# Kernel tuning notes

Hardware: AMD Instinct MI355X
Metric: run time of the kernel (lower is better)

The kernel has to match this reference:

```python
import jax, jax.numpy as jnp
import numpy as np

NEG_SLOPE = 0.2
BN_EPS = 1e-5


def _gatv2(x, Wl, Wr, att, b, src, dst, N):
    # PyG GATv2Conv, concat=False: lin_l on source, lin_r on target,
    # e = a^T LeakyReLU(x_l[j] + x_r[i]); softmax over incoming edges of i;
    # out = mean_h( sum_j alpha_ij * x_l[j] ) + bias
    H, C = att.shape
    xl = (x @ Wl).reshape(N, H, C)
    xr = (x @ Wr).reshape(N, H, C)
    e = jax.nn.leaky_relu(xl[src] + xr[dst], NEG_SLOPE)          # [E,H,C]
    score = jnp.einsum('ehc,hc->eh', e, att)                     # [E,H]
    m = jax.ops.segment_max(score, dst, num_segments=N)          # [N,H]
    a = jnp.exp(score - m[dst])
    denom = jax.ops.segment_sum(a, dst, num_segments=N)
    alpha = a / denom[dst]                                       # [E,H]
    out = jax.ops.segment_sum(alpha[..., None] * xl[src], dst, num_segments=N)  # [N,H,C]
    return out.mean(axis=1) + b


def _bn(h, g, be):
    # BatchNorm1d, training-mode statistics (biased variance)
    mu = h.mean(axis=0)
    var = h.var(axis=0)
    return g * (h - mu) * jax.lax.rsqrt(var + BN_EPS) + be


def _gelu(x):
    return jax.nn.gelu(x, approximate=False)


def setup_inputs() -> dict:
    key = jax.random.key(0)
    N, F, HID, LAT, H, E, G = 50000, 64, 64, 64, 4, 800000, 256
    ks = jax.random.split(key, 32)
    d = {}
    d['x'] = jax.random.normal(ks[0], (N, F), dtype=jnp.float32)
    d['edge_src'] = jax.random.randint(ks[1], (E,), 0, N, dtype=jnp.int32)
    d['edge_dst'] = jax.random.randint(ks[2], (E,), 0, N, dtype=jnp.int32)
    d['batch'] = jnp.sort(jax.random.randint(ks[3], (N,), 0, G, dtype=jnp.int32))
    d['num_graphs'] = G
    def lin(k, fi, fo):
        return jax.random.normal(k, (fi, fo), dtype=jnp.float32) / np.sqrt(fi)
    i = 4
    for L, fin in zip((1, 2, 3), (F, HID, HID)):
        d[f'Wl{L}'] = lin(ks[i], fin, H * HID); i += 1
        d[f'Wr{L}'] = lin(ks[i], fin, H * HID); i += 1
        d[f'att{L}'] = jax.random.normal(ks[i], (H, HID), dtype=jnp.float32) / np.sqrt(HID); i += 1
        d[f'b{L}'] = jnp.zeros((HID,), dtype=jnp.float32)
        d[f'g{L}'] = jax.random.uniform(ks[i], (HID,), dtype=jnp.float32, minval=0.5, maxval=1.5); i += 1
        d[f'be{L}'] = 0.1 * jax.random.normal(ks[i], (HID,), dtype=jnp.float32); i += 1
    d['Wmu'] = lin(ks[i], HID, LAT); i += 1
    d['bmu'] = jnp.zeros((LAT,), dtype=jnp.float32)
    d['Wlv'] = lin(ks[i], HID, LAT); i += 1
    d['blv'] = jnp.zeros((LAT,), dtype=jnp.float32)
    return d


def reference(x, edge_src, edge_dst, batch, num_graphs,
              Wl1, Wr1, att1, b1, g1, be1,
              Wl2, Wr2, att2, b2, g2, be2,
              Wl3, Wr3, att3, b3, g3, be3,
              Wmu, bmu, Wlv, blv):
    N = x.shape[0]
    loops = jnp.arange(N, dtype=edge_src.dtype)
    src = jnp.concatenate([edge_src, loops])  # add_self_loops=True (PyG default)
    dst = jnp.concatenate([edge_dst, loops])

    h = _gelu(_bn(_gatv2(x, Wl1, Wr1, att1, b1, src, dst, N), g1, be1))
    h_in = h
    h = _gelu(_bn(_gatv2(h, Wl2, Wr2, att2, b2, src, dst, N), g2, be2)) + h_in
    h_in = h
    h = _gelu(_bn(_gatv2(h, Wl3, Wr3, att3, b3, src, dst, N), g3, be3)) + h_in

    h_pool = jax.ops.segment_sum(h, batch, num_segments=num_graphs)  # global_add_pool
    return (h_pool @ Wmu + bmu, h_pool @ Wlv + blv)
```

## Files before the change

kernel.cpp:

```cpp
#include <hip/hip_runtime.h>
#include <math.h>

typedef __attribute__((ext_vector_type(8))) short bf16x8;
typedef __attribute__((ext_vector_type(4))) float f32x4;
typedef __attribute__((ext_vector_type(2))) float f32x2;

static __device__ __forceinline__ unsigned short f2bf(float f) {
  unsigned u = __float_as_uint(f);
  unsigned r = (u + 0x7FFF + ((u >> 16) & 1)) >> 16;
  return (unsigned short)r;
}

#define DPP_ADD(x, ctrl) \
  ((x) + __int_as_float(__builtin_amdgcn_update_dpp(0, __float_as_int(x), (ctrl), 0xf, 0xf, true)))

#define NSHARD 64
#define NEB 256
#define ECAP 6144


__global__ __launch_bounds__(256) void k_prep(const float* __restrict__ W0, const float* __restrict__ W1,
                                              const float* __restrict__ W2, const float* __restrict__ W3,
                                              const float* __restrict__ W4, const float* __restrict__ W5,
                                              unsigned short* __restrict__ wt,
                                              const int* __restrict__ esrc,
                                              const int* __restrict__ edst,
                                              int* __restrict__ bktcnt,
                                              int2* __restrict__ ebuf, int E, int N) {
  if (blockIdx.x < 384) {
    int gid = blockIdx.x * 256 + threadIdx.x;
    int m = gid >> 14;
    int r = gid & 16383;
    int k = r >> 8;
    int n = r & 255;
    const float* W = (m == 0) ? W0 : (m == 1) ? W1 : (m == 2) ? W2
                   : (m == 3) ? W3 : (m == 4) ? W4 : W5;
    wt[(size_t)m * 16384 + n * 64 + k] = f2bf(W[k * 256 + n]);
    return;
  }
  const int b = blockIdx.x - 384;
  const int nbk = (N + 255) >> 8;
  __shared__ int cnt[256], base[256];
  cnt[threadIdx.x] = 0;
  __syncthreads();
  const int chunk = (E + NEB - 1) / NEB;
  const int e0 = b * chunk, e1 = min(e0 + chunk, E);
  for (int e = e0 + threadIdx.x; e < e1; e += 256) atomicAdd(&cnt[edst[e] >> 8], 1);
  __syncthreads();
  if (threadIdx.x < nbk && cnt[threadIdx.x])
    base[threadIdx.x] = atomicAdd(&bktcnt[threadIdx.x], cnt[threadIdx.x]);
  cnt[threadIdx.x] = 0;
  __syncthreads();
  for (int e = e0 + threadIdx.x; e < e1; e += 256) {
    int d = edst[e];
    int bk = d >> 8;
    int p = base[bk] + atomicAdd(&cnt[bk], 1);
    ebuf[(size_t)bk * ECAP + p] = make_int2(d, esrc[e]);
  }
}


static __device__ __forceinline__ void csr_pass2(const int2* __restrict__ ebuf,
                                                 const int* __restrict__ bktcnt,
                                                 int* __restrict__ rowptr,
                                                 int* __restrict__ colb,
                                                 int* __restrict__ ccur,
                                                 int N, char* smem) {
  const int b = blockIdx.x;
  const int nbk = (N + 255) >> 8;
  if (b >= nbk) return;
  int* hist = (int*)smem;
  int* s = (int*)smem + 256;
  int* sb = (int*)smem + 512;
  const int tid = threadIdx.x;
  const int lo = b * ECAP;
  const int hi = lo + bktcnt[b];
  hist[tid] = 0;
  __syncthreads();
  for (int i = lo + tid; i < hi; i += 256) atomicAdd(&hist[ebuf[i].x & 255], 1);
  __syncthreads();
  int deg = hist[tid];
  int pd = (deg + 3) & ~3;
  s[tid] = pd;
  __syncthreads();
  for (int off = 1; off < 256; off <<= 1) {
    int t = (tid >= off) ? s[tid - off] : 0;
    __syncthreads();
    s[tid] += t;
    __syncthreads();
  }
  if (tid == 255) sb[0] = atomicAdd(ccur, s[255]);
  __syncthreads();
  int pos = sb[0] + s[tid] - pd;
  int node = (b << 8) + tid;
  if (node < N) rowptr[node] = (int)((unsigned)pos | ((unsigned)deg << 22));
  hist[tid] = pos;
  __syncthreads();
  for (int i = lo + tid; i < hi; i += 256) {
    int2 e = ebuf[i];
    int p = atomicAdd(&hist[e.x & 255], 1);
    colb[p] = e.y << 8;
  }
}


static __device__ __forceinline__ void mm_gemm(const float* __restrict__ src,
                                               const float* __restrict__ bnsums,
                                               const float* __restrict__ g,
                                               const float* __restrict__ be,
                                               const float* __restrict__ resid,
                                               float* __restrict__ hout,
                                               const unsigned short* __restrict__ wt,
                                               unsigned char* __restrict__ xlb,
                                               unsigned char* __restrict__ xrb,
                                               int N, int ntiles, float inv_n,
                                               char* smem) {
  unsigned short* Bs = (unsigned short*)smem;
  unsigned short* Ah = (unsigned short*)(smem + 32768);
  const int t = threadIdx.x;
  const unsigned short* wb = wt + (blockIdx.y ? 16384 : 0);
  unsigned char* dst = blockIdx.y ? xrb : xlb;

  const int wave = t >> 6, lane = t & 63;
  const int rw = (wave & 1) * 16, cw = (wave >> 1) * 128;
  const int m15 = lane & 15, quad = lane >> 4;
  const int arow = t >> 3, ac0 = (t & 7) * 8;
  const int aoff = arow * 64 + (((t & 7) ^ (arow & 7)) << 3);

  float scale[8], shift[8];
  if (bnsums) {
    float* stat = (float*)smem;
    if (t < 128) {
      float a = 0.f;
#pragma unroll
      for (int sd = 0; sd < NSHARD; ++sd) a += bnsums[sd * 128 + t];
      stat[t] = a;
    }
    __syncthreads();
#pragma unroll
    for (int i = 0; i < 8; ++i) {
      int c = ac0 + i;
      float mu = stat[c] * inv_n;
      float var = stat[64 + c] * inv_n - mu * mu;
      float rs = rsqrtf(var + 1e-5f) * g[c];
      scale[i] = rs;
      shift[i] = be[c] - mu * rs;
    }
    __syncthreads();
  }

#pragma unroll
  for (int j = 0; j < 8; ++j) {
    int cidx = t + 256 * j;
    int n = cidx >> 3, gg = cidx & 7;
    *(bf16x8*)&Bs[n * 64 + (((gg ^ ((n >> 3) & 7))) << 3)] =
        *(const bf16x8*)(wb + (size_t)n * 64 + gg * 8);
  }

  const bool wr_h = (hout != nullptr) && (blockIdx.y == 0);
  const int gstride = gridDim.x;

  float4 a0, a1, rv0, rv1;
  auto loadA = [&](int tl, float4& x0, float4& x1, float4& r0v, float4& r1v) {
    x0 = make_float4(0.f, 0.f, 0.f, 0.f);
    x1 = make_float4(0.f, 0.f, 0.f, 0.f);
    r0v = make_float4(0.f, 0.f, 0.f, 0.f);
    r1v = make_float4(0.f, 0.f, 0.f, 0.f);
    int gr = tl * 32 + arow;
    if (tl < ntiles && gr < N) {
      x0 = *(const float4*)(src + (size_t)gr * 64 + ac0);
      x1 = *(const float4*)(src + (size_t)gr * 64 + ac0 + 4);
      if (resid) {
        r0v = *(const float4*)(resid + (size_t)gr * 64 + ac0);
        r1v = *(const float4*)(resid + (size_t)gr * 64 + ac0 + 4);
      }
    }
  };
  loadA(blockIdx.x, a0, a1, rv0, rv1);

  for (int tile = blockIdx.x; tile < ntiles; tile += gstride) {
    int r0 = tile * 32;
    int gr = r0 + arow;
    {
      float vs[8] = {a0.x, a0.y, a0.z, a0.w, a1.x, a1.y, a1.z, a1.w};
      if (bnsums) {
        float rv[8] = {rv0.x, rv0.y, rv0.z, rv0.w, rv1.x, rv1.y, rv1.z, rv1.w};
#pragma unroll
        for (int i = 0; i < 8; ++i) {
          float v = fmaf(vs[i], scale[i], shift[i]);
          float ge = 0.5f * v * (1.f + erff(v * 0.70710678118654752f));
          vs[i] = ge + rv[i];
        }
        if (wr_h && gr < N) {
          float4 o0 = {vs[0], vs[1], vs[2], vs[3]};
          float4 o1 = {vs[4], vs[5], vs[6], vs[7]};
          *(float4*)(hout + (size_t)gr * 64 + ac0) = o0;
          *(float4*)(hout + (size_t)gr * 64 + ac0 + 4) = o1;
        }
      }
      bf16x8 hi8;
#pragma unroll
      for (int i = 0; i < 8; ++i) hi8[i] = (short)f2bf(vs[i]);
      *(bf16x8*)&Ah[aoff] = hi8;
    }
    __syncthreads();

    loadA(tile + gstride, a0, a1, rv0, rv1);

    f32x4 acc[8];
#pragma unroll
    for (int s = 0; s < 8; ++s) acc[s] = (f32x4){0.f, 0.f, 0.f, 0.f};
    const int xq = m15 & 7;
#pragma unroll
    for (int kk = 0; kk < 64; kk += 32) {
      const int ga = (((kk >> 3) + quad) ^ xq) << 3;
      bf16x8 ah = *(const bf16x8*)&Ah[(rw + m15) * 64 + ga];
#pragma unroll
      for (int s = 0; s < 8; ++s) {
        bf16x8 b = *(const bf16x8*)&Bs[(cw + m15 * 8 + s) * 64 + ga];
        acc[s] = __builtin_amdgcn_mfma_f32_16x16x32_bf16(ah, b, acc[s], 0, 0, 0);
      }
    }
#pragma unroll
    for (int r = 0; r < 4; ++r) {
      int row_g = r0 + rw + quad * 4 + r;
      if (row_g < N) {
        int w0 = __builtin_amdgcn_cvt_pk_fp8_f32(acc[0][r], acc[1][r], 0, false);
        w0 = __builtin_amdgcn_cvt_pk_fp8_f32(acc[2][r], acc[3][r], w0, true);
        int w1 = __builtin_amdgcn_cvt_pk_fp8_f32(acc[4][r], acc[5][r], 0, false);
        w1 = __builtin_amdgcn_cvt_pk_fp8_f32(acc[6][r], acc[7][r], w1, true);
        uint2 o = {(unsigned)w0, (unsigned)w1};
        *(uint2*)(dst + (size_t)row_g * 256 + cw + m15 * 8) = o;
      }
    }
    __syncthreads();
  }
}

__global__ __launch_bounds__(256, 4) void k_mm0(const float* __restrict__ src,
                                                const unsigned short* __restrict__ wt,
                                                unsigned char* __restrict__ xlb,
                                                unsigned char* __restrict__ xrb,
                                                const int2* __restrict__ ebuf,
                                                const int* __restrict__ bktcnt,
                                                int* __restrict__ rowptr,
                                                int* __restrict__ colb,
                                                int* __restrict__ ccur,
                                                int N, int ntiles) {
  __shared__ __align__(16) char smem[36864];
  if (blockIdx.y == 2) {
    csr_pass2(ebuf, bktcnt, rowptr, colb, ccur, N, smem);
    return;
  }
  mm_gemm(src, nullptr, nullptr, nullptr, nullptr, nullptr, wt, xlb, xrb, N, ntiles, 0.f, smem);
}

__global__ __launch_bounds__(256, 4) void k_mm1(const float* __restrict__ src,
                                                const float* __restrict__ bnsums,
                                                const float* __restrict__ g,
                                                const float* __restrict__ be,
                                                float* __restrict__ hout,
                                                const unsigned short* __restrict__ wt,
                                                unsigned char* __restrict__ xlb,
                                                unsigned char* __restrict__ xrb,
                                                int N, int ntiles, float inv_n) {
  __shared__ __align__(16) char smem[36864];
  mm_gemm(src, bnsums, g, be, nullptr, hout, wt, xlb, xrb, N, ntiles, inv_n, smem);
}

__global__ __launch_bounds__(256, 4) void k_mm2(const float* __restrict__ src,
                                                const float* __restrict__ bnsums,
                                                const float* __restrict__ g,
                                                const float* __restrict__ be,
                                                const float* __restrict__ resid,
                                                float* __restrict__ hout,
                                                const unsigned short* __restrict__ wt,
                                                unsigned char* __restrict__ xlb,
                                                unsigned char* __restrict__ xrb,
                                                int N, int ntiles, float inv_n) {
  __shared__ __align__(16) char smem[36864];
  mm_gemm(src, bnsums, g, be, resid, hout, wt, xlb, xrb, N, ntiles, inv_n, smem);
}


static __device__ __forceinline__ void gat_body(const unsigned char* __restrict__ xlb,
                                                const unsigned char* __restrict__ xrb,
                                                const float* __restrict__ att,
                                                const float* __restrict__ bias,
                                                const int* __restrict__ rowptr,
                                                const int* __restrict__ colb,
                                                float* __restrict__ out,
                                                float* __restrict__ bnsums, int N) {
  __shared__ float sres[4][64];
  const int lane = threadIdx.x & 63;
  const int wv = threadIdx.x >> 6;
  const int node0 = blockIdx.x * 4 + wv;
  const bool valid = node0 < N;
  const int node = __builtin_amdgcn_readfirstlane(valid ? node0 : 0);
  const int rp = rowptr[node];
  const int beg = rp & 0x3FFFFF;
  const int deg = (int)(((unsigned)rp) >> 22);
  const int end = valid ? beg + deg : beg;

  const unsigned char* xl = xlb;
  const unsigned lb = (unsigned)lane * 4u;

  int4 c0 = *(const int4*)(colb + beg);
  int4 c1 = *(const int4*)(colb + beg + 4);
  unsigned vbs = *(const unsigned*)(xl + ((unsigned)(node << 8) + lb));
  unsigned d0 = *(const unsigned*)(xl + ((unsigned)c0.x + lb));
  unsigned d1 = *(const unsigned*)(xl + ((unsigned)c0.y + lb));
  unsigned d2 = *(const unsigned*)(xl + ((unsigned)c0.z + lb));
  unsigned d3 = *(const unsigned*)(xl + ((unsigned)c0.w + lb));
  unsigned t0 = *(const unsigned*)(xl + ((unsigned)c1.x + lb));
  unsigned t1 = *(const unsigned*)(xl + ((unsigned)c1.y + lb));
  unsigned t2 = *(const unsigned*)(xl + ((unsigned)c1.z + lb));
  unsigned t3 = *(const unsigned*)(xl + ((unsigned)c1.w + lb));
  int4 cn = *(const int4*)(colb + beg + 8);

  float4 a4 = *(const float4*)(att + lane * 4);
  const float LOG2E = 1.4426950408889634f;
  const f32x2 a01 = {a4.x * LOG2E, a4.y * LOG2E};
  const f32x2 a23 = {a4.z * LOG2E, a4.w * LOG2E};
  const f32x2 c02 = {0.2f, 0.2f};
  unsigned xru = *(const unsigned*)(xrb + ((unsigned)(node << 8) + lb));
  const f32x2 xr01 = __builtin_amdgcn_cvt_pk_f32_fp8((int)xru, false);
  const f32x2 xr23 = __builtin_amdgcn_cvt_pk_f32_fp8((int)xru, true);
  const f32x2 sv01 = __builtin_amdgcn_cvt_pk_f32_fp8((int)vbs, false);
  const f32x2 sv23 = __builtin_amdgcn_cvt_pk_f32_fp8((int)vbs, true);

  float m;
  {
    f32x2 s01 = sv01 + xr01;
    f32x2 s23 = sv23 + xr23;
    s01 = __builtin_elementwise_max(s01, s01 * c02);
    s23 = __builtin_elementwise_max(s23, s23 * c02);
    f32x2 q = __builtin_elementwise_fma(s23, a23, s01 * a01);
    float p = q.x + q.y;
    p = DPP_ADD(p, 0xB1);
    p = DPP_ADD(p, 0x4E);
    p = DPP_ADD(p, 0x124);
    p = DPP_ADD(p, 0x128);
    m = p;
  }
  float lsum = 1.f;
  f32x2 o01 = sv01, o23 = sv23;

  auto proc = [&](unsigned vb, bool ok) {
    f32x2 v01 = __builtin_amdgcn_cvt_pk_f32_fp8((int)vb, false);
    f32x2 v23 = __builtin_amdgcn_cvt_pk_f32_fp8((int)vb, true);
    f32x2 s01 = v01 + xr01;
    f32x2 s23 = v23 + xr23;
    s01 = __builtin_elementwise_max(s01, s01 * c02);
    s23 = __builtin_elementwise_max(s23, s23 * c02);
    f32x2 q = __builtin_elementwise_fma(s23, a23, s01 * a01);
    float p = q.x + q.y;
    p = DPP_ADD(p, 0xB1);
    p = DPP_ADD(p, 0x4E);
    p = DPP_ADD(p, 0x124);
    p = DPP_ADD(p, 0x128);
    float w = __builtin_amdgcn_exp2f(fminf(p - m, 126.f));
    w = ok ? w : 0.f;
    lsum += w;
    f32x2 w2 = {w, w};
    o01 = __builtin_elementwise_fma(w2, v01, o01);
    o23 = __builtin_elementwise_fma(w2, v23, o23);
  };

  for (int e = beg; e < end; e += 4) {
    unsigned u0 = *(const unsigned*)(xl + ((unsigned)cn.x + lb));
    unsigned u1 = *(const unsigned*)(xl + ((unsigned)cn.y + lb));
    unsigned u2 = *(const unsigned*)(xl + ((unsigned)cn.z + lb));
    unsigned u3 = *(const unsigned*)(xl + ((unsigned)cn.w + lb));
    cn = *(const int4*)(colb + e + 12);
    proc(d0, true);
    proc(d1, e + 1 < end);
    proc(d2, e + 2 < end);
    proc(d3, e + 3 < end);
    d0 = t0; d1 = t1; d2 = t2; d3 = t3;
    t0 = u0; t1 = u1; t2 = u2; t3 = u3;
  }

  float inv = __builtin_amdgcn_rcpf(lsum);
  float rx = o01.x * inv, ry = o01.y * inv, rz = o23.x * inv, rw2 = o23.y * inv;
  rx += __shfl_xor(rx, 16, 64); rx += __shfl_xor(rx, 32, 64);
  ry += __shfl_xor(ry, 16, 64); ry += __shfl_xor(ry, 32, 64);
  rz += __shfl_xor(rz, 16, 64); rz += __shfl_xor(rz, 32, 64);
  rw2 += __shfl_xor(rw2, 16, 64); rw2 += __shfl_xor(rw2, 32, 64);
  if (lane < 16) {
    float4 res = {0.f, 0.f, 0.f, 0.f};
    if (valid) {
      float4 b4 = *(const float4*)(bias + lane * 4);
      res.x = 0.25f * rx + b4.x;
      res.y = 0.25f * ry + b4.y;
      res.z = 0.25f * rz + b4.z;
      res.w = 0.25f * rw2 + b4.w;
      *(float4*)(out + (size_t)node * 64 + lane * 4) = res;
    }
    *(float4*)&sres[wv][lane * 4] = res;
  }
  __syncthreads();
  if (threadIdx.x < 64) {
    int c = threadIdx.x;
    float s0 = sres[0][c], s1 = sres[1][c], s2 = sres[2][c], s3 = sres[3][c];
    float* bs = bnsums + (size_t)(blockIdx.x & (NSHARD - 1)) * 128;
    atomicAdd(&bs[c], s0 + s1 + s2 + s3);
    atomicAdd(&bs[64 + c], s0 * s0 + s1 * s1 + s2 * s2 + s3 * s3);
  }
}

__global__ __launch_bounds__(256) void k_gat0(const unsigned char* __restrict__ xlb,
                                              const unsigned char* __restrict__ xrb,
                                              const float* __restrict__ att,
                                              const float* __restrict__ bias,
                                              const int* __restrict__ rowptr,
                                              const int* __restrict__ colb,
                                              float* __restrict__ out,
                                              float* __restrict__ bnsums, int N) {
  gat_body(xlb, xrb, att, bias, rowptr, colb, out, bnsums, N);
}
__global__ __launch_bounds__(256) void k_gat1(const unsigned char* __restrict__ xlb,
                                              const unsigned char* __restrict__ xrb,
                                              const float* __restrict__ att,
                                              const float* __restrict__ bias,
                                              const int* __restrict__ rowptr,
                                              const int* __restrict__ colb,
                                              float* __restrict__ out,
                                              float* __restrict__ bnsums, int N) {
  gat_body(xlb, xrb, att, bias, rowptr, colb, out, bnsums, N);
}
__global__ __launch_bounds__(256) void k_gat2(const unsigned char* __restrict__ xlb,
                                              const unsigned char* __restrict__ xrb,
                                              const float* __restrict__ att,
                                              const float* __restrict__ bias,
                                              const int* __restrict__ rowptr,
                                              const int* __restrict__ colb,
                                              float* __restrict__ out,
                                              float* __restrict__ bnsums, int N) {
  gat_body(xlb, xrb, att, bias, rowptr, colb, out, bnsums, N);
}


__global__ __launch_bounds__(256) void k_bn_pool(const float* __restrict__ gat,
                                                 const float* __restrict__ bnsums,
                                                 const float* __restrict__ g,
                                                 const float* __restrict__ be,
                                                 const float* __restrict__ resid,
                                                 const int* __restrict__ batch,
                                                 float* __restrict__ pool,
                                                 int N, float inv_n) {
  __shared__ float sc[64], sh[64];
  if (threadIdx.x < 64) {
    int c = threadIdx.x;
    float s = 0.f, q = 0.f;
    for (int sd = 0; sd < NSHARD; ++sd) {
      s += bnsums[sd * 128 + c];
      q += bnsums[sd * 128 + 64 + c];
    }
    float mu = s * inv_n;
    float var = q * inv_n - mu * mu;
    float rs = rsqrtf(var + 1e-5f) * g[c];
    sc[c] = rs;
    sh[c] = be[c] - mu * rs;
  }
  __syncthreads();
  const int c = threadIdx.x & 63;
  const int wv = threadIdx.x >> 6;
  int n0 = (blockIdx.x * 4 + wv) * 32;
  if (n0 >= N) return;
  int n1 = min(n0 + 32, N);
  int curg = batch[n0];
  float acc = 0.f;
  for (int n = n0; n < n1; ++n) {
    int b = batch[n];
    if (b != curg) {
      atomicAdd(&pool[(size_t)curg * 64 + c], acc);
      acc = 0.f;
      curg = b;
    }
    float v = fmaf(gat[(size_t)n * 64 + c], sc[c], sh[c]);
    float ge = 0.5f * v * (1.f + erff(v * 0.70710678118654752f));
    acc += ge + resid[(size_t)n * 64 + c];
  }
  atomicAdd(&pool[(size_t)curg * 64 + c], acc);
}


__global__ void k_head(const float* __restrict__ pool, const float* __restrict__ Wmu,
                       const float* __restrict__ bmu, const float* __restrict__ Wlv,
                       const float* __restrict__ blv, float* __restrict__ out, int G) {
  int g = blockIdx.x;
  int c = threadIdx.x;
  __shared__ float row[64];
  row[c] = pool[(size_t)g * 64 + c];
  __syncthreads();
  float am = 0.f, al = 0.f;
  for (int k = 0; k < 64; ++k) {
    float r = row[k];
    am = fmaf(r, Wmu[k * 64 + c], am);
    al = fmaf(r, Wlv[k * 64 + c], al);
  }
  out[(size_t)g * 64 + c] = am + bmu[c];
  out[(size_t)G * 64 + (size_t)g * 64 + c] = al + blv[c];
}


extern "C" void kernel_launch(void* const* d_in, const int* in_sizes, int n_in,
                              void* d_out, int out_size, void* d_ws, size_t ws_size,
                              hipStream_t stream) {
  const float* x    = (const float*)d_in[0];
  const int* esrc   = (const int*)d_in[1];
  const int* edst   = (const int*)d_in[2];
  const int* batch  = (const int*)d_in[3];
  const float* Wl[3]  = {(const float*)d_in[5],  (const float*)d_in[11], (const float*)d_in[17]};
  const float* Wr[3]  = {(const float*)d_in[6],  (const float*)d_in[12], (const float*)d_in[18]};
  const float* att[3] = {(const float*)d_in[7],  (const float*)d_in[13], (const float*)d_in[19]};
  const float* bia[3] = {(const float*)d_in[8],  (const float*)d_in[14], (const float*)d_in[20]};
  const float* gam[3] = {(const float*)d_in[9],  (const float*)d_in[15], (const float*)d_in[21]};
  const float* bet[3] = {(const float*)d_in[10], (const float*)d_in[16], (const float*)d_in[22]};
  const float* Wmu = (const float*)d_in[23];
  const float* bmu = (const float*)d_in[24];
  const float* Wlv = (const float*)d_in[25];
  const float* blv = (const float*)d_in[26];
  float* out = (float*)d_out;

  const int N = in_sizes[0] / 64;
  const int E = in_sizes[1];
  const int G = out_size / 128;
  const int nbk = (N + 255) / 256;

  char* p = (char*)d_ws;
  auto alloc = [&](size_t bytes) -> void* {
    void* r = (void*)p;
    p += (bytes + 255) & ~(size_t)255;
    return r;
  };
  int*   bktcnt  = (int*)alloc(256 * 4);
  float* bnsums  = (float*)alloc(3 * NSHARD * 128 * 4);
  float* pool    = (float*)alloc((size_t)G * 64 * 4);
  int*   ccur    = (int*)alloc(256);
  int*   colb    = (int*)alloc(((size_t)E + 3 * (size_t)N + 64) * 4);
  char*  zend    = p;
  unsigned char* xlb = (unsigned char*)alloc((size_t)N * 256);
  unsigned char* xrb = (unsigned char*)alloc((size_t)N * 256);
  float* hA     = (float*)alloc((size_t)N * 64 * 4);
  float* hB     = (float*)alloc((size_t)N * 64 * 4);
  float* gat    = (float*)alloc((size_t)N * 64 * 4);
  int*   rowptr = (int*)alloc((size_t)(N + 1) * 4);
  int2*  ebuf   = (int2*)alloc((size_t)nbk * ECAP * 8);
  unsigned short* wt = (unsigned short*)alloc(6 * 16384 * 2);

  const int nbGat = (N + 3) / 4;
  const int ntiles = (N + 31) / 32;
  const float inv_n = 1.f / (float)N;

  hipMemsetAsync(bktcnt, 0, (size_t)(zend - (char*)bktcnt), stream);

  k_prep<<<384 + NEB, 256, 0, stream>>>(Wl[0], Wr[0], Wl[1], Wr[1], Wl[2], Wr[2], wt,
                                        esrc, edst, bktcnt, ebuf, E, N);

  float* bns0 = bnsums;
  float* bns1 = bnsums + NSHARD * 128;
  float* bns2 = bnsums + 2 * NSHARD * 128;

  k_mm0<<<dim3(512, 3), 256, 0, stream>>>(x, wt, xlb, xrb, ebuf, bktcnt, rowptr, colb,
                                          ccur, N, ntiles);
  k_gat0<<<nbGat, 256, 0, stream>>>(xlb, xrb, att[0], bia[0], rowptr, colb, gat, bns0, N);
  k_mm1<<<dim3(512, 2), 256, 0, stream>>>(gat, bns0, gam[0], bet[0], hA,
                                          wt + 2 * 16384, xlb, xrb, N, ntiles, inv_n);
  k_gat1<<<nbGat, 256, 0, stream>>>(xlb, xrb, att[1], bia[1], rowptr, colb, gat, bns1, N);
  k_mm2<<<dim3(512, 2), 256, 0, stream>>>(gat, bns1, gam[1], bet[1], hA, hB,
                                          wt + 4 * 16384, xlb, xrb, N, ntiles, inv_n);
  k_gat2<<<nbGat, 256, 0, stream>>>(xlb, xrb, att[2], bia[2], rowptr, colb, gat, bns2, N);
  k_bn_pool<<<(N + 127) / 128, 256, 0, stream>>>(gat, bns2, gam[2], bet[2], hB, batch, pool,
                                                 N, inv_n);
  k_head<<<G, 64, 0, stream>>>(pool, Wmu, bmu, Wlv, blv, out, G);
}
```

Measured before the change: 365.1 us.

## Split GAT aggregation wave into two half-waves each handling alternate edges

The GAT gather kernel now has each 32-lane half of a wavefront process a different edge, with every lane holding 8 fp8 features (uint2 loads) instead of 4. This halves the number of serial per-edge score/exp/FMA steps per wave and shortens the per-head reduction by one DPP step, at the cost of more registers per lane, an extra cross-half merge of lsum and outputs, and a longer final shuffle reduction. Masking uses per-half edge validity, and the self-loop term is counted only in the lower half.

```diff
diff --git a/kernel.cpp b/kernel.cpp
--- a/kernel.cpp
+++ b/kernel.cpp
@@ -294,6 +294,8 @@
   __shared__ float sres[4][64];
   const int lane = threadIdx.x & 63;
   const int wv = threadIdx.x >> 6;
+  const int half = lane >> 5;
+  const int l5 = lane & 31;
   const int node0 = blockIdx.x * 4 + wv;
   const bool valid = node0 < N;
   const int node = __builtin_amdgcn_readfirstlane(valid ? node0 : 0);
@@ -303,101 +305,117 @@
   const int end = valid ? beg + deg : beg;
 
   const unsigned char* xl = xlb;
-  const unsigned lb = (unsigned)lane * 4u;
+  const unsigned lb = (unsigned)l5 * 8u;
+
+  auto sel = [&](int a, int b) { return (unsigned)(half ? b : a); };
 
   int4 c0 = *(const int4*)(colb + beg);
   int4 c1 = *(const int4*)(colb + beg + 4);
-  unsigned vbs = *(const unsigned*)(xl + ((unsigned)(node << 8) + lb));
-  unsigned d0 = *(const unsigned*)(xl + ((unsigned)c0.x + lb));
-  unsigned d1 = *(const unsigned*)(xl + ((unsigned)c0.y + lb));
-  unsigned d2 = *(const unsigned*)(xl + ((unsigned)c0.z + lb));
-  unsigned d3 = *(const unsigned*)(xl + ((unsigned)c0.w + lb));
-  unsigned t0 = *(const unsigned*)(xl + ((unsigned)c1.x + lb));
-  unsigned t1 = *(const unsigned*)(xl + ((unsigned)c1.y + lb));
-  unsigned t2 = *(const unsigned*)(xl + ((unsigned)c1.z + lb));
-  unsigned t3 = *(const unsigned*)(xl + ((unsigned)c1.w + lb));
+  const unsigned self_off = (unsigned)(node << 8);
+  uint2 vbs = *(const uint2*)(xl + self_off + lb);
+  uint2 pd0 = *(const uint2*)(xl + (sel(c0.x, c0.y) + lb));
+  uint2 pd1 = *(const uint2*)(xl + (sel(c0.z, c0.w) + lb));
+  uint2 pt0 = *(const uint2*)(xl + (sel(c1.x, c1.y) + lb));
+  uint2 pt1 = *(const uint2*)(xl + (sel(c1.z, c1.w) + lb));
   int4 cn = *(const int4*)(colb + beg + 8);
 
-  float4 a4 = *(const float4*)(att + lane * 4);
+  float4 aa = *(const float4*)(att + l5 * 8);
+  float4 ab = *(const float4*)(att + l5 * 8 + 4);
   const float LOG2E = 1.4426950408889634f;
-  const f32x2 a01 = {a4.x * LOG2E, a4.y * LOG2E};
-  const f32x2 a23 = {a4.z * LOG2E, a4.w * LOG2E};
+  const f32x2 a01 = {aa.x * LOG2E, aa.y * LOG2E};
+  const f32x2 a23 = {aa.z * LOG2E, aa.w * LOG2E};
+  const f32x2 a45 = {ab.x * LOG2E, ab.y * LOG2E};
+  const f32x2 a67 = {ab.z * LOG2E, ab.w * LOG2E};
   const f32x2 c02 = {0.2f, 0.2f};
-  unsigned xru = *(const unsigned*)(xrb + ((unsigned)(node << 8) + lb));
-  const f32x2 xr01 = __builtin_amdgcn_cvt_pk_f32_fp8((int)xru, false);
-  const f32x2 xr23 = __builtin_amdgcn_cvt_pk_f32_fp8((int)xru, true);
-  const f32x2 sv01 = __builtin_amdgcn_cvt_pk_f32_fp8((int)vbs, false);
-  const f32x2 sv23 = __builtin_amdgcn_cvt_pk_f32_fp8((int)vbs, true);
-
-  float m;
-  {
-    f32x2 s01 = sv01 + xr01;
-    f32x2 s23 = sv23 + xr23;
+  uint2 xru = *(const uint2*)(xrb + self_off + lb);
+  const f32x2 xr01 = __builtin_amdgcn_cvt_pk_f32_fp8((int)xru.x, false);
+  const f32x2 xr23 = __builtin_amdgcn_cvt_pk_f32_fp8((int)xru.x, true);
+  const f32x2 xr45 = __builtin_amdgcn_cvt_pk_f32_fp8((int)xru.y, false);
+  const f32x2 xr67 = __builtin_amdgcn_cvt_pk_f32_fp8((int)xru.y, true);
+
+  auto score = [&](uint2 vb, f32x2& v01, f32x2& v23, f32x2& v45, f32x2& v67) -> float {
+    v01 = __builtin_amdgcn_cvt_pk_f32_fp8((int)vb.x, false);
+    v23 = __builtin_amdgcn_cvt_pk_f32_fp8((int)vb.x, true);
+    v45 = __builtin_amdgcn_cvt_pk_f32_fp8((int)vb.y, false);
+    v67 = __builtin_amdgcn_cvt_pk_f32_fp8((int)vb.y, true);
+    f32x2 s01 = v01 + xr01;
+    f32x2 s23 = v23 + xr23;
+    f32x2 s45 = v45 + xr45;
+    f32x2 s67 = v67 + xr67;
     s01 = __builtin_elementwise_max(s01, s01 * c02);
     s23 = __builtin_elementwise_max(s23, s23 * c02);
-    f32x2 q = __builtin_elementwise_fma(s23, a23, s01 * a01);
+    s45 = __builtin_elementwise_max(s45, s45 * c02);
+    s67 = __builtin_elementwise_max(s67, s67 * c02);
+    f32x2 q = s01 * a01;
+    q = __builtin_elementwise_fma(s23, a23, q);
+    q = __builtin_elementwise_fma(s45, a45, q);
+    q = __builtin_elementwise_fma(s67, a67, q);
     float p = q.x + q.y;
     p = DPP_ADD(p, 0xB1);
     p = DPP_ADD(p, 0x4E);
-    p = DPP_ADD(p, 0x124);
-    p = DPP_ADD(p, 0x128);
-    m = p;
-  }
-  float lsum = 1.f;
-  f32x2 o01 = sv01, o23 = sv23;
-
-  auto proc = [&](unsigned vb, bool ok) {
-    f32x2 v01 = __builtin_amdgcn_cvt_pk_f32_fp8((int)vb, false);
-    f32x2 v23 = __builtin_amdgcn_cvt_pk_f32_fp8((int)vb, true);
-    f32x2 s01 = v01 + xr01;
-    f32x2 s23 = v23 + xr23;
-    s01 = __builtin_elementwise_max(s01, s01 * c02);
-    s23 = __builtin_elementwise_max(s23, s23 * c02);
-    f32x2 q = __builtin_elementwise_fma(s23, a23, s01 * a01);
-    float p = q.x + q.y;
-    p = DPP_ADD(p, 0xB1);
-    p = DPP_ADD(p, 0x4E);
-    p = DPP_ADD(p, 0x124);
-    p = DPP_ADD(p, 0x128);
+    p = DPP_ADD(p, 0x141);
+    return p;
+  };
+
+  f32x2 sv01, sv23, sv45, sv67;
+  const float m = score(vbs, sv01, sv23, sv45, sv67);
+
+  const float hsel = half ? 0.f : 1.f;
+  float lsum = hsel;
+  const f32x2 hs2 = {hsel, hsel};
+  f32x2 o01 = sv01 * hs2, o23 = sv23 * hs2, o45 = sv45 * hs2, o67 = sv67 * hs2;
+
+  auto proc = [&](uint2 vb, int ebase) {
+    f32x2 v01, v23, v45, v67;
+    float p = score(vb, v01, v23, v45, v67);
     float w = __builtin_amdgcn_exp2f(fminf(p - m, 126.f));
-    w = ok ? w : 0.f;
+    w = (ebase + half < end) ? w : 0.f;
     lsum += w;
     f32x2 w2 = {w, w};
     o01 = __builtin_elementwise_fma(w2, v01, o01);
     o23 = __builtin_elementwise_fma(w2, v23, o23);
+    o45 = __builtin_elementwise_fma(w2, v45, o45);
+    o67 = __builtin_elementwise_fma(w2, v67, o67);
   };
 
   for (int e = beg; e < end; e += 4) {
-    unsigned u0 = *(const unsigned*)(xl + ((unsigned)cn.x + lb));
-    unsigned u1 = *(const unsigned*)(xl + ((unsigned)cn.y + lb));
-    unsigned u2 = *(const unsigned*)(xl + ((unsigned)cn.z + lb));
-    unsigned u3 = *(const unsigned*)(xl + ((unsigned)cn.w + lb));
+    uint2 pu0 = *(const uint2*)(xl + (sel(cn.x, cn.y) + lb));
+    uint2 pu1 = *(const uint2*)(xl + (sel(cn.z, cn.w) + lb));
     cn = *(const int4*)(colb + e + 12);
-    proc(d0, true);
-    proc(d1, e + 1 < end);
-    proc(d2, e + 2 < end);
-    proc(d3, e + 3 < end);
-    d0 = t0; d1 = t1; d2 = t2; d3 = t3;
-    t0 = u0; t1 = u1; t2 = u2; t3 = u3;
-  }
-
+    proc(pd0, e);
+    proc(pd1, e + 2);
+    pd0 = pt0; pd1 = pt1;
+    pt0 = pu0; pt1 = pu1;
+  }
+
+  lsum += __shfl_xor(lsum, 32, 64);
   float inv = __builtin_amdgcn_rcpf(lsum);
-  float rx = o01.x * inv, ry = o01.y * inv, rz = o23.x * inv, rw2 = o23.y * inv;
-  rx += __shfl_xor(rx, 16, 64); rx += __shfl_xor(rx, 32, 64);
-  ry += __shfl_xor(ry, 16, 64); ry += __shfl_xor(ry, 32, 64);
-  rz += __shfl_xor(rz, 16, 64); rz += __shfl_xor(rz, 32, 64);
-  rw2 += __shfl_xor(rw2, 16, 64); rw2 += __shfl_xor(rw2, 32, 64);
-  if (lane < 16) {
-    float4 res = {0.f, 0.f, 0.f, 0.f};
+  float r[8] = {o01.x * inv, o01.y * inv, o23.x * inv, o23.y * inv,
+                o45.x * inv, o45.y * inv, o67.x * inv, o67.y * inv};
+#pragma unroll
+  for (int j = 0; j < 8; ++j) {
+    r[j] += __shfl_xor(r[j], 8, 64);
+    r[j] += __shfl_xor(r[j], 16, 64);
+    r[j] += __shfl_xor(r[j], 32, 64);
+  }
+  if (lane < 8) {
+    float4 res0 = {0.f, 0.f, 0.f, 0.f}, res1 = {0.f, 0.f, 0.f, 0.f};
     if (valid) {
-      float4 b4 = *(const float4*)(bias + lane * 4);
-      res.x = 0.25f * rx + b4.x;
-      res.y = 0.25f * ry + b4.y;
-      res.z = 0.25f * rz + b4.z;
-      res.w = 0.25f * rw2 + b4.w;
-      *(float4*)(out + (size_t)node * 64 + lane * 4) = res;
-    }
-    *(float4*)&sres[wv][lane * 4] = res;
+      float4 b0 = *(const float4*)(bias + lane * 8);
+      float4 b1 = *(const float4*)(bias + lane * 8 + 4);
+      res0.x = 0.25f * r[0] + b0.x;
+      res0.y = 0.25f * r[1] + b0.y;
+      res0.z = 0.25f * r[2] + b0.z;
+      res0.w = 0.25f * r[3] + b0.w;
+      res1.x = 0.25f * r[4] + b1.x;
+      res1.y = 0.25f * r[5] + b1.y;
+      res1.z = 0.25f * r[6] + b1.z;
+      res1.w = 0.25f * r[7] + b1.w;
+      *(float4*)(out + (size_t)node * 64 + lane * 8) = res0;
+      *(float4*)(out + (size_t)node * 64 + lane * 8 + 4) = res1;
+    }
+    *(float4*)&sres[wv][lane * 8] = res0;
+    *(float4*)&sres[wv][lane * 8 + 4] = res1;
   }
   __syncthreads();
   if (threadIdx.x < 64) {
```

Measured after the change: 358.1 us (median of 2 runs). No clear change (-1.9%).
